# Optimization experiments

Hardware: AMD Instinct MI355X
Metric: run time of the kernel (lower is better)

Reference implementation:

```python
import jax, jax.numpy as jnp
import numpy as np

NEG_SLOPE = 0.2  # PyG GATConv default


def _gat_layer(x, src, dst, W, a_src, a_dst, b, heads, concat):
    # x: [N, F_in], W: [F_in, H*C], a_src/a_dst: [H, C], b: [H*C] or [C]
    N = x.shape[0]
    h = (x @ W).reshape(N, heads, -1)                      # [N, H, C]
    s_n = jnp.sum(h * a_src, axis=-1)                      # [N, H] per-node src score
    d_n = jnp.sum(h * a_dst, axis=-1)                      # [N, H] per-node dst score
    e = jax.nn.leaky_relu(s_n[src] + d_n[dst], NEG_SLOPE)  # [E, H] edge logits
    # segment softmax over incoming edges of each destination node
    m = jax.ops.segment_max(e, dst, num_segments=N)        # [N, H]
    ex = jnp.exp(e - m[dst])                               # [E, H]
    denom = jax.ops.segment_sum(ex, dst, num_segments=N)   # [N, H]
    alpha = ex / denom[dst]                                # [E, H]
    out = jax.ops.segment_sum(h[src] * alpha[:, :, None], dst, num_segments=N)  # [N, H, C]
    if concat:
        out = out.reshape(N, -1)
    else:
        out = out.mean(axis=1)
    return out + b


def setup_inputs() -> dict:
    key = jax.random.key(0)
    ks = jax.random.split(key, 12)
    N, E = 50000, 800000
    F_in, Ch, H, F_out = 128, 32, 4, 64
    x = jax.random.normal(ks[0], (N, F_in), dtype=jnp.float32)
    edge_index = jax.random.randint(ks[1], (2, E), 0, N, dtype=jnp.int64)
    # layer 1 params (glorot-ish scale)
    W1 = jax.random.normal(ks[2], (F_in, H * Ch), dtype=jnp.float32) * (1.0 / np.sqrt(F_in))
    a1_src = jax.random.normal(ks[3], (H, Ch), dtype=jnp.float32) * (1.0 / np.sqrt(Ch))
    a1_dst = jax.random.normal(ks[4], (H, Ch), dtype=jnp.float32) * (1.0 / np.sqrt(Ch))
    b1 = jnp.zeros((H * Ch,), dtype=jnp.float32)
    # layer 2 params (heads=1)
    W2 = jax.random.normal(ks[5], (H * Ch, F_out), dtype=jnp.float32) * (1.0 / np.sqrt(H * Ch))
    a2_src = jax.random.normal(ks[6], (1, F_out), dtype=jnp.float32) * (1.0 / np.sqrt(F_out))
    a2_dst = jax.random.normal(ks[7], (1, F_out), dtype=jnp.float32) * (1.0 / np.sqrt(F_out))
    b2 = jnp.zeros((F_out,), dtype=jnp.float32)
    return {"x": x, "edge_index": edge_index, "drpt": 0,
            "W1": W1, "a1_src": a1_src, "a1_dst": a1_dst, "b1": b1,
            "W2": W2, "a2_src": a2_src, "a2_dst": a2_dst, "b2": b2}


def reference(x, edge_index, drpt, W1, a1_src, a1_dst, b1, W2, a2_src, a2_dst, b2):
    N = x.shape[0]
    # PyG GATConv adds self-loops by default
    loops = jnp.arange(N, dtype=edge_index.dtype)
    src = jnp.concatenate([edge_index[0], loops])
    dst = jnp.concatenate([edge_index[1], loops])
    h = _gat_layer(x, src, dst, W1, a1_src, a1_dst, b1, heads=4, concat=True)
    h = jax.nn.relu(h)
    # F.dropout with training=False (eval) is identity; drpt unused at inference
    out = _gat_layer(h, src, dst, W2, a2_src, a2_dst, b2, heads=1, concat=True)
    return out
```

## Files before the change

### kernel.cpp

```cpp
#include <hip/hip_runtime.h>
#include <hip/hip_fp16.h>


typedef _Float16 half8 __attribute__((ext_vector_type(8)));
typedef float f32x4 __attribute__((ext_vector_type(4)));

constexpr int BCAP = 8192;
constexpr int NTHB = 256;

__global__ __launch_bounds__(256) void zero_gcur(int* __restrict__ gcur, int nb) {
    int i = blockIdx.x * blockDim.x + threadIdx.x;
    if (i < nb) gcur[i] = 0;
}

__global__ __launch_bounds__(256) void bin_edges(const int* __restrict__ ei,
                                                 int* __restrict__ gcur,
                                                 unsigned int* __restrict__ packed,
                                                 int E, int nb) {
    __shared__ int cnt[256];
    __shared__ int base[256];
    const int tid = threadIdx.x;
    if (tid < nb) cnt[tid] = 0;
    __syncthreads();

    const int e0 = blockIdx.x * 2048;
    int src[8], dst[8], rk[8];
    #pragma unroll
    for (int j = 0; j < 8; ++j) {
        int e = e0 + tid + j * 256;
        if (e < E) {
            src[j] = ei[e];
            dst[j] = ei[E + e];
            rk[j]  = atomicAdd(&cnt[dst[j] >> 8], 1);
        } else dst[j] = -1;
    }
    __syncthreads();
    if (tid < nb) base[tid] = cnt[tid] ? atomicAdd(&gcur[tid], cnt[tid]) : 0;
    __syncthreads();
    #pragma unroll
    for (int j = 0; j < 8; ++j) {
        if (dst[j] >= 0) {
            int b = dst[j] >> 8;
            int pos = base[b] + rk[j];
            if (pos > BCAP - 1) pos = BCAP - 1;
            unsigned int pk = ((unsigned)(dst[j] & 255) << 16) | (unsigned)src[j];
            packed[(size_t)b * BCAP + pos] = pk;
        }
    }
}

__global__ __launch_bounds__(256) void scan_buckets(const int* __restrict__ gcur,
                                                    int* __restrict__ bbase,
                                                    int nb, int N) {
    __shared__ int s[256];
    int tid = threadIdx.x;
    int nodes = N - tid * NTHB;
    nodes = nodes < 0 ? 0 : (nodes > NTHB ? NTHB : nodes);
    int v = (tid < nb) ? gcur[tid] + nodes : 0;
    s[tid] = v;
    __syncthreads();
    for (int off = 1; off < 256; off <<= 1) {
        int t = (tid >= off) ? s[tid - off] : 0;
        __syncthreads();
        s[tid] += t;
        __syncthreads();
    }
    if (tid < nb) bbase[tid] = s[tid] - v;
}

__global__ __launch_bounds__(256) void build_csr(const unsigned int* __restrict__ packed,
                                                 const int* __restrict__ gcur,
                                                 const int* __restrict__ bbase,
                                                 unsigned short* __restrict__ csr,
                                                 int* __restrict__ row_end,
                                                 int N) {
    __shared__ int deg[256];
    __shared__ int scn[256];
    __shared__ unsigned short lcsr[BCAP + 256];
    const int b   = blockIdx.x;
    const int tid = threadIdx.x;
    const int ne  = gcur[b];
    const int node = (b << 8) + tid;
    const bool real = node < N;

    deg[tid] = real ? 1 : 0;
    __syncthreads();

    const unsigned int* pk = &packed[(size_t)b * BCAP];
    for (int k = tid; k < ne; k += 256)
        atomicAdd(&deg[pk[k] >> 16], 1);
    __syncthreads();

    int v = deg[tid];
    scn[tid] = v;
    __syncthreads();
    for (int off = 1; off < 256; off <<= 1) {
        int t = (tid >= off) ? scn[tid - off] : 0;
        __syncthreads();
        scn[tid] += t;
        __syncthreads();
    }
    const int incl  = scn[tid];
    const int start = incl - v;
    const int tot   = scn[255];
    const int gbase = bbase[b];
    __syncthreads();

    if (real) {
        lcsr[start] = (unsigned short)node;
        row_end[node] = gbase + incl;
    }
    deg[tid] = start + (real ? 1 : 0);
    __syncthreads();

    for (int k = tid; k < ne; k += 256) {
        unsigned int p = pk[k];
        int pos = atomicAdd(&deg[p >> 16], 1);
        lcsr[pos] = (unsigned short)(p & 0xffffu);
    }
    __syncthreads();

    for (int k = tid; k < tot; k += 256)
        csr[gbase + k] = lcsr[k];
}

__global__ __launch_bounds__(256) void prep_wt(const float* __restrict__ W1,
                                               const float* __restrict__ W2,
                                               _Float16* __restrict__ Wt1,
                                               _Float16* __restrict__ Wt2) {
    int i = blockIdx.x * blockDim.x + threadIdx.x;
    if (i < 128 * 128) {
        int c = i >> 7, k = i & 127;
        Wt1[i] = (_Float16)W1[k * 128 + c];
    } else if (i < 128 * 128 + 64 * 128) {
        int j = i - 128 * 128;
        int c = j >> 7, k = j & 127;
        Wt2[j] = (_Float16)W2[k * 64 + c];
    }
}

template<int FOUT, int H, typename TIN>
__global__ __launch_bounds__(256) void gemm_score_mfma(const TIN* __restrict__ X,
                                                       const _Float16* __restrict__ Wt,
                                                       const float* __restrict__ a_src,
                                                       const float* __restrict__ a_dst,
                                                       _Float16* __restrict__ Yh,
                                                       float* __restrict__ s,
                                                       float* __restrict__ d, int N) {
    constexpr int NT  = FOUT / 16;
    constexpr int TPH = NT / H;
    __shared__ _Float16 xs[64][136];

    const int tid  = threadIdx.x;
    const int row0 = blockIdx.x * 64;

    if constexpr (sizeof(TIN) == 4) {
        for (int c = tid; c < 2048; c += 256) {
            int r = c >> 5, c4 = c & 31;
            float4 v = make_float4(0.f, 0.f, 0.f, 0.f);
            if (row0 + r < N)
                v = reinterpret_cast<const float4*>(X)[(size_t)(row0 + r) * 32 + c4];
            _Float16* p = &xs[r][c4 * 4];
            p[0] = (_Float16)v.x; p[1] = (_Float16)v.y;
            p[2] = (_Float16)v.z; p[3] = (_Float16)v.w;
        }
    } else {
        for (int c = tid; c < 1024; c += 256) {
            int r = c >> 4, c8 = c & 15;
            uint4 v = make_uint4(0, 0, 0, 0);
            if (row0 + r < N)
                v = reinterpret_cast<const uint4*>(X)[(size_t)(row0 + r) * 16 + c8];
            *reinterpret_cast<uint4*>(&xs[r][c8 * 8]) = v;
        }
    }
    __syncthreads();

    const int wid  = tid >> 6;
    const int lane = tid & 63;
    const int l15  = lane & 15;
    const int lg   = lane >> 4;

    f32x4 acc[NT];
    #pragma unroll
    for (int n = 0; n < NT; ++n) acc[n] = (f32x4){0.f, 0.f, 0.f, 0.f};

    const half8* WtV = reinterpret_cast<const half8*>(Wt);
    #pragma unroll
    for (int ks = 0; ks < 4; ++ks) {
        half8 a = *reinterpret_cast<const half8*>(&xs[wid * 16 + l15][ks * 32 + lg * 8]);
        #pragma unroll
        for (int n = 0; n < NT; ++n) {
            half8 b = WtV[(size_t)(n * 16 + l15) * 16 + ks * 4 + lg];
            acc[n] = __builtin_amdgcn_mfma_f32_16x16x32_f16(a, b, acc[n], 0, 0, 0);
        }
    }

    float av[NT], bv[NT];
    #pragma unroll
    for (int n = 0; n < NT; ++n) {
        av[n] = a_src[n * 16 + l15];
        bv[n] = a_dst[n * 16 + l15];
    }

    #pragma unroll
    for (int r = 0; r < 4; ++r) {
        int row = row0 + wid * 16 + lg * 4 + r;
        bool ok = row < N;
        if (ok) {
            #pragma unroll
            for (int n = 0; n < NT; ++n)
                Yh[(size_t)row * FOUT + n * 16 + l15] = (_Float16)acc[n][r];
        }
        #pragma unroll
        for (int h = 0; h < H; ++h) {
            float ls = 0.f, ld = 0.f;
            #pragma unroll
            for (int t = 0; t < TPH; ++t) {
                int n = h * TPH + t;
                ls = fmaf(acc[n][r], av[n], ls);
                ld = fmaf(acc[n][r], bv[n], ld);
            }
            #pragma unroll
            for (int m = 1; m < 16; m <<= 1) {
                ls += __shfl_xor(ls, m);
                ld += __shfl_xor(ld, m);
            }
            if (ok && l15 == h) {
                s[(size_t)row * H + h] = ls;
                d[(size_t)row * H + h] = ld;
            }
        }
    }
}

__device__ __forceinline__ float edge_w(float x) {
    return __expf(x > 0.f ? x : 0.2f * x);
}

__device__ __forceinline__ void acc8(float* acc, uint4 r, float w) {
    const __half2* h2 = reinterpret_cast<const __half2*>(&r);
    #pragma unroll
    for (int j = 0; j < 4; ++j) {
        float2 f = __half22float2(h2[j]);
        acc[2 * j]     = fmaf(w, f.x, acc[2 * j]);
        acc[2 * j + 1] = fmaf(w, f.y, acc[2 * j + 1]);
    }
}

template<int H, int C, bool RELU, bool OUTH>
__global__ __launch_bounds__(256) void gat_gather(const unsigned short* __restrict__ csr,
                                                  const int* __restrict__ row_end,
                                                  const float* __restrict__ s,
                                                  const float* __restrict__ d,
                                                  const _Float16* __restrict__ hh,
                                                  const float* __restrict__ b,
                                                  void* __restrict__ outp, int N) {
    constexpr int CT = H * C;
    constexpr int G  = CT / 8;
    int t = blockIdx.x * blockDim.x + threadIdx.x;
    int node = t / G;
    int lane = t % G;
    if (node >= N) return;

    int start = node ? row_end[node - 1] : 0;
    int end   = row_end[node];

    int c0 = lane * 8;
    int head = c0 / C;
    float dn = d[(size_t)node * H + head];

    float acc[8] = {0.f, 0.f, 0.f, 0.f, 0.f, 0.f, 0.f, 0.f};
    float den = 0.f;

    for (int k = start; k < end; k += 8) {
        int idx[8];
        float sv[8];
        uint4 rr[8];
        #pragma unroll
        for (int j = 0; j < 8; ++j) {
            int kk = k + j;
            int kc = kk < end ? kk : end - 1;
            idx[j] = csr[kc];
            sv[j]  = s[(size_t)idx[j] * H + head];
        }
        #pragma unroll
        for (int j = 0; j < 8; ++j)
            rr[j] = *reinterpret_cast<const uint4*>(&hh[(size_t)idx[j] * CT + c0]);
        #pragma unroll
        for (int j = 0; j < 8; ++j) {
            float w = edge_w(sv[j] + dn);
            if (k + j >= end) w = 0.f;
            den += w;
            acc8(acc, rr[j], w);
        }
    }

    float inv = 1.f / den;
    float o[8];
    #pragma unroll
    for (int j = 0; j < 8; ++j) {
        o[j] = acc[j] * inv + b[c0 + j];
        if (RELU) o[j] = fmaxf(o[j], 0.f);
    }
    if constexpr (OUTH) {
        union { _Float16 h[8]; uint4 u; } pk;
        #pragma unroll
        for (int j = 0; j < 8; ++j) pk.h[j] = (_Float16)o[j];
        _Float16* out = (_Float16*)outp;
        *reinterpret_cast<uint4*>(&out[(size_t)node * CT + c0]) = pk.u;
    } else {
        float* out = (float*)outp;
        float4* op = reinterpret_cast<float4*>(&out[(size_t)node * CT + c0]);
        op[0] = make_float4(o[0], o[1], o[2], o[3]);
        op[1] = make_float4(o[4], o[5], o[6], o[7]);
    }
}

extern "C" void kernel_launch(void* const* d_in, const int* in_sizes, int n_in,
                              void* d_out, int out_size, void* d_ws, size_t ws_size,
                              hipStream_t stream) {
    const float* x      = (const float*)d_in[0];
    const int*   ei     = (const int*)d_in[1];
    const float* W1     = (const float*)d_in[3];
    const float* a1_src = (const float*)d_in[4];
    const float* a1_dst = (const float*)d_in[5];
    const float* b1     = (const float*)d_in[6];
    const float* W2     = (const float*)d_in[7];
    const float* a2_src = (const float*)d_in[8];
    const float* a2_dst = (const float*)d_in[9];
    const float* b2     = (const float*)d_in[10];

    const int N = in_sizes[0] / 128;
    const int E = in_sizes[1] / 2;
    const int NB = (N + NTHB - 1) / NTHB;
    float* out = (float*)d_out;

    float* f = (float*)d_ws;
    _Float16* h1h = (_Float16*)f;
    _Float16* x2h = (_Float16*)(f + (size_t)N * 64);
    unsigned int* packed = (unsigned int*)x2h;
    float* s1 = f + (size_t)N * 128;
    float* d1 = f + (size_t)N * 132;
    int*   row_end = (int*)(f + (size_t)N * 136);
    int*   gcur    = row_end + N;
    int*   bbase   = gcur + 256;
    _Float16* Wt1  = (_Float16*)(bbase + 256);
    _Float16* Wt2  = Wt1 + 128 * 128;
    unsigned short* csr = (unsigned short*)(Wt2 + 64 * 128);
    _Float16* h2h = h1h;
    float* s2 = s1;
    float* d2 = d1;

    zero_gcur<<<1, 256, 0, stream>>>(gcur, NB);
    bin_edges<<<(E + 2047) / 2048, 256, 0, stream>>>(ei, gcur, packed, E, NB);
    scan_buckets<<<1, 256, 0, stream>>>(gcur, bbase, NB, N);
    build_csr<<<NB, 256, 0, stream>>>(packed, gcur, bbase, csr, row_end, N);
    prep_wt<<<96, 256, 0, stream>>>(W1, W2, Wt1, Wt2);

    gemm_score_mfma<128, 4, float><<<(N + 63) / 64, 256, 0, stream>>>(
        x, Wt1, a1_src, a1_dst, h1h, s1, d1, N);
    gat_gather<4, 32, true, true><<<(int)(((size_t)N * 16 + 255) / 256), 256, 0, stream>>>(
        csr, row_end, s1, d1, h1h, b1, x2h, N);

    gemm_score_mfma<64, 1, _Float16><<<(N + 63) / 64, 256, 0, stream>>>(
        x2h, Wt2, a2_src, a2_dst, h2h, s2, d2, N);
    gat_gather<1, 64, false, false><<<(int)(((size_t)N * 8 + 255) / 256), 256, 0, stream>>>(
        csr, row_end, s2, d2, h2h, b2, out, N);
}
```

Measured before the change: 128.7 us.

## Fuse edge binning with first GEMM and fold bucket scan into CSR build

Merges the edge binning kernel and the layer-1 GEMM/score kernel into one grid, with block index choosing the role, so the two independent stages overlap. The gcur zeroing moves into prep_wt, and the global bucket prefix scan is recomputed redundantly inside each build_csr block instead of in a separate single-block kernel. This removes three kernel launches and their serialization gaps. The cost is a redundant per-block scan and a larger shared-memory footprint for the fused kernel.

```diff
diff --git a/kernel.cpp b/kernel.cpp
--- a/kernel.cpp
+++ b/kernel.cpp
@@ -7,127 +7,12 @@
 
 constexpr int BCAP = 8192;
 constexpr int NTHB = 256;
-
-__global__ __launch_bounds__(256) void zero_gcur(int* __restrict__ gcur, int nb) {
-    int i = blockIdx.x * blockDim.x + threadIdx.x;
-    if (i < nb) gcur[i] = 0;
-}
-
-__global__ __launch_bounds__(256) void bin_edges(const int* __restrict__ ei,
-                                                 int* __restrict__ gcur,
-                                                 unsigned int* __restrict__ packed,
-                                                 int E, int nb) {
-    __shared__ int cnt[256];
-    __shared__ int base[256];
-    const int tid = threadIdx.x;
-    if (tid < nb) cnt[tid] = 0;
-    __syncthreads();
-
-    const int e0 = blockIdx.x * 2048;
-    int src[8], dst[8], rk[8];
-    #pragma unroll
-    for (int j = 0; j < 8; ++j) {
-        int e = e0 + tid + j * 256;
-        if (e < E) {
-            src[j] = ei[e];
-            dst[j] = ei[E + e];
-            rk[j]  = atomicAdd(&cnt[dst[j] >> 8], 1);
-        } else dst[j] = -1;
-    }
-    __syncthreads();
-    if (tid < nb) base[tid] = cnt[tid] ? atomicAdd(&gcur[tid], cnt[tid]) : 0;
-    __syncthreads();
-    #pragma unroll
-    for (int j = 0; j < 8; ++j) {
-        if (dst[j] >= 0) {
-            int b = dst[j] >> 8;
-            int pos = base[b] + rk[j];
-            if (pos > BCAP - 1) pos = BCAP - 1;
-            unsigned int pk = ((unsigned)(dst[j] & 255) << 16) | (unsigned)src[j];
-            packed[(size_t)b * BCAP + pos] = pk;
-        }
-    }
-}
-
-__global__ __launch_bounds__(256) void scan_buckets(const int* __restrict__ gcur,
-                                                    int* __restrict__ bbase,
-                                                    int nb, int N) {
-    __shared__ int s[256];
-    int tid = threadIdx.x;
-    int nodes = N - tid * NTHB;
-    nodes = nodes < 0 ? 0 : (nodes > NTHB ? NTHB : nodes);
-    int v = (tid < nb) ? gcur[tid] + nodes : 0;
-    s[tid] = v;
-    __syncthreads();
-    for (int off = 1; off < 256; off <<= 1) {
-        int t = (tid >= off) ? s[tid - off] : 0;
-        __syncthreads();
-        s[tid] += t;
-        __syncthreads();
-    }
-    if (tid < nb) bbase[tid] = s[tid] - v;
-}
-
-__global__ __launch_bounds__(256) void build_csr(const unsigned int* __restrict__ packed,
-                                                 const int* __restrict__ gcur,
-                                                 const int* __restrict__ bbase,
-                                                 unsigned short* __restrict__ csr,
-                                                 int* __restrict__ row_end,
-                                                 int N) {
-    __shared__ int deg[256];
-    __shared__ int scn[256];
-    __shared__ unsigned short lcsr[BCAP + 256];
-    const int b   = blockIdx.x;
-    const int tid = threadIdx.x;
-    const int ne  = gcur[b];
-    const int node = (b << 8) + tid;
-    const bool real = node < N;
-
-    deg[tid] = real ? 1 : 0;
-    __syncthreads();
-
-    const unsigned int* pk = &packed[(size_t)b * BCAP];
-    for (int k = tid; k < ne; k += 256)
-        atomicAdd(&deg[pk[k] >> 16], 1);
-    __syncthreads();
-
-    int v = deg[tid];
-    scn[tid] = v;
-    __syncthreads();
-    for (int off = 1; off < 256; off <<= 1) {
-        int t = (tid >= off) ? scn[tid - off] : 0;
-        __syncthreads();
-        scn[tid] += t;
-        __syncthreads();
-    }
-    const int incl  = scn[tid];
-    const int start = incl - v;
-    const int tot   = scn[255];
-    const int gbase = bbase[b];
-    __syncthreads();
-
-    if (real) {
-        lcsr[start] = (unsigned short)node;
-        row_end[node] = gbase + incl;
-    }
-    deg[tid] = start + (real ? 1 : 0);
-    __syncthreads();
-
-    for (int k = tid; k < ne; k += 256) {
-        unsigned int p = pk[k];
-        int pos = atomicAdd(&deg[p >> 16], 1);
-        lcsr[pos] = (unsigned short)(p & 0xffffu);
-    }
-    __syncthreads();
-
-    for (int k = tid; k < tot; k += 256)
-        csr[gbase + k] = lcsr[k];
-}
 
 __global__ __launch_bounds__(256) void prep_wt(const float* __restrict__ W1,
                                                const float* __restrict__ W2,
                                                _Float16* __restrict__ Wt1,
-                                               _Float16* __restrict__ Wt2) {
+                                               _Float16* __restrict__ Wt2,
+                                               int* __restrict__ gcur) {
     int i = blockIdx.x * blockDim.x + threadIdx.x;
     if (i < 128 * 128) {
         int c = i >> 7, k = i & 127;
@@ -136,42 +21,66 @@
         int j = i - 128 * 128;
         int c = j >> 7, k = j & 127;
         Wt2[j] = (_Float16)W2[k * 64 + c];
-    }
-}
-
-template<int FOUT, int H, typename TIN>
-__global__ __launch_bounds__(256) void gemm_score_mfma(const TIN* __restrict__ X,
-                                                       const _Float16* __restrict__ Wt,
-                                                       const float* __restrict__ a_src,
-                                                       const float* __restrict__ a_dst,
-                                                       _Float16* __restrict__ Yh,
-                                                       float* __restrict__ s,
-                                                       float* __restrict__ d, int N) {
-    constexpr int NT  = FOUT / 16;
-    constexpr int TPH = NT / H;
-    __shared__ _Float16 xs[64][136];
-
-    const int tid  = threadIdx.x;
-    const int row0 = blockIdx.x * 64;
-
-    if constexpr (sizeof(TIN) == 4) {
-        for (int c = tid; c < 2048; c += 256) {
-            int r = c >> 5, c4 = c & 31;
-            float4 v = make_float4(0.f, 0.f, 0.f, 0.f);
-            if (row0 + r < N)
-                v = reinterpret_cast<const float4*>(X)[(size_t)(row0 + r) * 32 + c4];
-            _Float16* p = &xs[r][c4 * 4];
-            p[0] = (_Float16)v.x; p[1] = (_Float16)v.y;
-            p[2] = (_Float16)v.z; p[3] = (_Float16)v.w;
-        }
-    } else {
-        for (int c = tid; c < 1024; c += 256) {
-            int r = c >> 4, c8 = c & 15;
-            uint4 v = make_uint4(0, 0, 0, 0);
-            if (row0 + r < N)
-                v = reinterpret_cast<const uint4*>(X)[(size_t)(row0 + r) * 16 + c8];
-            *reinterpret_cast<uint4*>(&xs[r][c8 * 8]) = v;
-        }
+    } else if (i < 128 * 128 + 64 * 128 + 256) {
+        gcur[i - (128 * 128 + 64 * 128)] = 0;
+    }
+}
+
+__global__ __launch_bounds__(256) void fused_bin_gemm1(
+        const int* __restrict__ ei, int* __restrict__ gcur,
+        unsigned int* __restrict__ packed, int E, int nb, int nbin,
+        const float* __restrict__ X, const _Float16* __restrict__ Wt,
+        const float* __restrict__ a_src, const float* __restrict__ a_dst,
+        _Float16* __restrict__ Yh, float* __restrict__ s,
+        float* __restrict__ d, int N) {
+    __shared__ __align__(16) char smem[64 * 136 * 2];
+    const int tid = threadIdx.x;
+
+    if (blockIdx.x < nbin) {
+        int* cnt  = (int*)smem;
+        int* base = cnt + 256;
+        if (tid < nb) cnt[tid] = 0;
+        __syncthreads();
+
+        const int e0 = blockIdx.x * 2048;
+        int src[8], dst[8], rk[8];
+        #pragma unroll
+        for (int j = 0; j < 8; ++j) {
+            int e = e0 + tid + j * 256;
+            if (e < E) {
+                src[j] = ei[e];
+                dst[j] = ei[E + e];
+                rk[j]  = atomicAdd(&cnt[dst[j] >> 8], 1);
+            } else dst[j] = -1;
+        }
+        __syncthreads();
+        if (tid < nb) base[tid] = cnt[tid] ? atomicAdd(&gcur[tid], cnt[tid]) : 0;
+        __syncthreads();
+        #pragma unroll
+        for (int j = 0; j < 8; ++j) {
+            if (dst[j] >= 0) {
+                int b = dst[j] >> 8;
+                int pos = base[b] + rk[j];
+                if (pos > BCAP - 1) pos = BCAP - 1;
+                unsigned int pk = ((unsigned)(dst[j] & 255) << 16) | (unsigned)src[j];
+                packed[(size_t)b * BCAP + pos] = pk;
+            }
+        }
+        return;
+    }
+
+    constexpr int FOUT = 128, H = 4, NT = 8, TPH = 2;
+    auto xs = (_Float16(*)[136])smem;
+    const int row0 = (blockIdx.x - nbin) * 64;
+
+    for (int c = tid; c < 2048; c += 256) {
+        int r = c >> 5, c4 = c & 31;
+        float4 v = make_float4(0.f, 0.f, 0.f, 0.f);
+        if (row0 + r < N)
+            v = reinterpret_cast<const float4*>(X)[(size_t)(row0 + r) * 32 + c4];
+        _Float16* p = &xs[r][c4 * 4];
+        p[0] = (_Float16)v.x; p[1] = (_Float16)v.y;
+        p[2] = (_Float16)v.z; p[3] = (_Float16)v.w;
     }
     __syncthreads();
 
@@ -233,6 +142,147 @@
     }
 }
 
+__global__ __launch_bounds__(256) void build_csr(const unsigned int* __restrict__ packed,
+                                                 const int* __restrict__ gcur,
+                                                 unsigned short* __restrict__ csr,
+                                                 int* __restrict__ row_end,
+                                                 int N, int nb) {
+    __shared__ int deg[256];
+    __shared__ int scn[256];
+    __shared__ unsigned short lcsr[BCAP + 256];
+    const int b   = blockIdx.x;
+    const int tid = threadIdx.x;
+    const int ne  = gcur[b];
+    const int node = (b << 8) + tid;
+    const bool real = node < N;
+
+    int nodes_t = N - tid * NTHB;
+    nodes_t = nodes_t < 0 ? 0 : (nodes_t > NTHB ? NTHB : nodes_t);
+    int vall = (tid < nb) ? gcur[tid] + nodes_t : 0;
+    scn[tid] = vall;
+    __syncthreads();
+    for (int off = 1; off < 256; off <<= 1) {
+        int t = (tid >= off) ? scn[tid - off] : 0;
+        __syncthreads();
+        scn[tid] += t;
+        __syncthreads();
+    }
+    int nodes_b = N - b * NTHB;
+    nodes_b = nodes_b < 0 ? 0 : (nodes_b > NTHB ? NTHB : nodes_b);
+    const int gbase = scn[b] - ne - nodes_b;
+    __syncthreads();
+
+    deg[tid] = real ? 1 : 0;
+    __syncthreads();
+
+    const unsigned int* pk = &packed[(size_t)b * BCAP];
+    for (int k = tid; k < ne; k += 256)
+        atomicAdd(&deg[pk[k] >> 16], 1);
+    __syncthreads();
+
+    int v = deg[tid];
+    scn[tid] = v;
+    __syncthreads();
+    for (int off = 1; off < 256; off <<= 1) {
+        int t = (tid >= off) ? scn[tid - off] : 0;
+        __syncthreads();
+        scn[tid] += t;
+        __syncthreads();
+    }
+    const int incl  = scn[tid];
+    const int start = incl - v;
+    const int tot   = scn[255];
+    __syncthreads();
+
+    if (real) {
+        lcsr[start] = (unsigned short)node;
+        row_end[node] = gbase + incl;
+    }
+    deg[tid] = start + (real ? 1 : 0);
+    __syncthreads();
+
+    for (int k = tid; k < ne; k += 256) {
+        unsigned int p = pk[k];
+        int pos = atomicAdd(&deg[p >> 16], 1);
+        lcsr[pos] = (unsigned short)(p & 0xffffu);
+    }
+    __syncthreads();
+
+    for (int k = tid; k < tot; k += 256)
+        csr[gbase + k] = lcsr[k];
+}
+
+__global__ __launch_bounds__(256) void gemm_score2(const _Float16* __restrict__ X,
+                                                   const _Float16* __restrict__ Wt,
+                                                   const float* __restrict__ a_src,
+                                                   const float* __restrict__ a_dst,
+                                                   _Float16* __restrict__ Yh,
+                                                   float* __restrict__ s,
+                                                   float* __restrict__ d, int N) {
+    constexpr int FOUT = 64, NT = 4;
+    __shared__ _Float16 xs[64][136];
+    const int tid  = threadIdx.x;
+    const int row0 = blockIdx.x * 64;
+
+    for (int c = tid; c < 1024; c += 256) {
+        int r = c >> 4, c8 = c & 15;
+        uint4 v = make_uint4(0, 0, 0, 0);
+        if (row0 + r < N)
+            v = reinterpret_cast<const uint4*>(X)[(size_t)(row0 + r) * 16 + c8];
+        *reinterpret_cast<uint4*>(&xs[r][c8 * 8]) = v;
+    }
+    __syncthreads();
+
+    const int wid  = tid >> 6;
+    const int lane = tid & 63;
+    const int l15  = lane & 15;
+    const int lg   = lane >> 4;
+
+    f32x4 acc[NT];
+    #pragma unroll
+    for (int n = 0; n < NT; ++n) acc[n] = (f32x4){0.f, 0.f, 0.f, 0.f};
+
+    const half8* WtV = reinterpret_cast<const half8*>(Wt);
+    #pragma unroll
+    for (int ks = 0; ks < 4; ++ks) {
+        half8 a = *reinterpret_cast<const half8*>(&xs[wid * 16 + l15][ks * 32 + lg * 8]);
+        #pragma unroll
+        for (int n = 0; n < NT; ++n) {
+            half8 b = WtV[(size_t)(n * 16 + l15) * 16 + ks * 4 + lg];
+            acc[n] = __builtin_amdgcn_mfma_f32_16x16x32_f16(a, b, acc[n], 0, 0, 0);
+        }
+    }
+
+    float av[NT], bv[NT];
+    #pragma unroll
+    for (int n = 0; n < NT; ++n) {
+        av[n] = a_src[n * 16 + l15];
+        bv[n] = a_dst[n * 16 + l15];
+    }
+
+    #pragma unroll
+    for (int r = 0; r < 4; ++r) {
+        int row = row0 + wid * 16 + lg * 4 + r;
+        bool ok = row < N;
+        float ls = 0.f, ld = 0.f;
+        #pragma unroll
+        for (int n = 0; n < NT; ++n) {
+            if (ok) Yh[(size_t)row * FOUT + n * 16 + l15] = (_Float16)acc[n][r];
+            ls = fmaf(acc[n][r], av[n], ls);
+            ld = fmaf(acc[n][r], bv[n], ld);
+        }
+        #pragma unroll
+        for (int m = 1; m < 16; m <<= 1) {
+            ls += __shfl_xor(ls, m);
+            ld += __shfl_xor(ld, m);
+        }
+        if (ok && l15 == 0) {
+            s[row] = ls;
+            d[row] = ld;
+        }
+    }
+}
+
 __device__ __forceinline__ float edge_w(float x) {
     return __expf(x > 0.f ? x : 0.2f * x);
 }
@@ -333,6 +383,8 @@
     const int N = in_sizes[0] / 128;
     const int E = in_sizes[1] / 2;
     const int NB = (N + NTHB - 1) / NTHB;
+    const int NBIN = (E + 2047) / 2048;
+    const int NG1  = (N + 63) / 64;
     float* out = (float*)d_out;
 
     float* f = (float*)d_ws;
@@ -343,27 +395,21 @@
     float* d1 = f + (size_t)N * 132;
     int*   row_end = (int*)(f + (size_t)N * 136);
     int*   gcur    = row_end + N;
-    int*   bbase   = gcur + 256;
-    _Float16* Wt1  = (_Float16*)(bbase + 256);
+    _Float16* Wt1  = (_Float16*)(gcur + 256);
     _Float16* Wt2  = Wt1 + 128 * 128;
     unsigned short* csr = (unsigned short*)(Wt2 + 64 * 128);
     _Float16* h2h = h1h;
     float* s2 = s1;
     float* d2 = d1;
 
-    zero_gcur<<<1, 256, 0, stream>>>(gcur, NB);
-    bin_edges<<<(E + 2047) / 2048, 256, 0, stream>>>(ei, gcur, packed, E, NB);
-    scan_buckets<<<1, 256, 0, stream>>>(gcur, bbase, NB, N);
-    build_csr<<<NB, 256, 0, stream>>>(packed, gcur, bbase, csr, row_end, N);
-    prep_wt<<<96, 256, 0, stream>>>(W1, W2, Wt1, Wt2);
-
-    gemm_score_mfma<128, 4, float><<<(N + 63) / 64, 256, 0, stream>>>(
+    prep_wt<<<97, 256, 0, stream>>>(W1, W2, Wt1, Wt2, gcur);
+    fused_bin_gemm1<<<NBIN + NG1, 256, 0, stream>>>(
+        ei, gcur, packed, E, NB, NBIN,
         x, Wt1, a1_src, a1_dst, h1h, s1, d1, N);
+    build_csr<<<NB, 256, 0, stream>>>(packed, gcur, csr, row_end, N, NB);
     gat_gather<4, 32, true, true><<<(int)(((size_t)N * 16 + 255) / 256), 256, 0, stream>>>(
         csr, row_end, s1, d1, h1h, b1, x2h, N);
-
-    gemm_score_mfma<64, 1, _Float16><<<(N + 63) / 64, 256, 0, stream>>>(
-        x2h, Wt2, a2_src, a2_dst, h2h, s2, d2, N);
+    gemm_score2<<<NG1, 256, 0, stream>>>(x2h, Wt2, a2_src, a2_dst, h2h, s2, d2, N);
     gat_gather<1, 64, false, false><<<(int)(((size_t)N * 8 + 255) / 256), 256, 0, stream>>>(
         csr, row_end, s2, d2, h2h, b2, out, N);
 }
```

Result: faster. 118.5 us (-7.9%).
